# Optimization experiments

Hardware: AMD Instinct MI355X
Metric: run time of the kernel (lower is better)

## Reference

```python
import jax, jax.numpy as jnp
import numpy as np

B, C, H, W = 2, 192, 64, 64
NHEADS = 8


def setup_inputs() -> dict:
    key = jax.random.key(0)
    ks = jax.random.split(key, 6)
    L = H * W
    return {
        "x": jax.random.normal(ks[0], (B, C, H, W), dtype=jnp.float32),
        "mask": jax.random.normal(ks[1], (B, L, L), dtype=jnp.float32),
        "w_qkv": jax.random.normal(ks[2], (3 * C, C), dtype=jnp.float32) * (1.0 / np.sqrt(C)),
        "b_qkv": jax.random.normal(ks[3], (3 * C,), dtype=jnp.float32) * 0.02,
        "w_proj": jax.random.normal(ks[4], (C, C), dtype=jnp.float32) * (1.0 / np.sqrt(C)),
        "b_proj": jax.random.normal(ks[5], (C,), dtype=jnp.float32) * 0.02,
        "num_heads": NHEADS,
    }


def reference(x, mask, w_qkv, b_qkv, w_proj, b_proj, num_heads):
    b, c, h, w = x.shape
    L = h * w
    hd = c // num_heads  # head dim
    # 1x1 conv == per-pixel linear over channels
    qkv = jnp.einsum('bchw,oc->bohw', x, w_qkv) + b_qkv[None, :, None, None]
    q, k, v = jnp.split(qkv, 3, axis=1)  # each [b, c, h, w]

    def to_heads(t):
        # b (head hd) h w -> b head (h w) hd
        return t.reshape(b, num_heads, hd, L).transpose(0, 1, 3, 2)

    q, k, v = to_heads(q), to_heads(k), to_heads(v)
    scale = num_heads ** (-0.5)  # NOTE: original scales by num_heads, not head_dim
    attn = jnp.einsum('bnld,bnmd->bnlm', q, k) * scale + mask[:, None, :, :]
    attn = jax.nn.softmax(attn, axis=-1)
    out = jnp.einsum('bnlm,bnmd->bnld', attn, v)  # [b, head, L, hd]
    # b head L hd -> b (head hd) h w
    out = out.transpose(0, 1, 3, 2).reshape(b, c, h, w)
    out = jnp.einsum('bchw,oc->bohw', out, w_proj) + b_proj[None, :, None, None]
    return out
```

## Files before the change

### kernel.cpp

```cpp
#include <hip/hip_runtime.h>

#define B_  2
#define C_  192
#define L_  4096
#define NH_ 8
#define HD_ 24
#define C3_ 576
#define KV_ 64
#define NT_ (L_ / KV_)

typedef _Float16 f16;
typedef __attribute__((ext_vector_type(8))) f16 f16x8;
typedef __attribute__((ext_vector_type(16))) float f32x16;

__device__ __forceinline__ int pk2(float a, float b) {
    union { __fp16 h __attribute__((ext_vector_type(2))); int i; } u;
    u.h = __builtin_amdgcn_cvt_pkrtz(a, b);
    return u.i;
}
__device__ __forceinline__ int pk2_rte(float a, float b) {
    union { f16 h[2]; int i; } u;
    u.h[0] = (f16)a; u.h[1] = (f16)b;
    return u.i;
}

union Frag { f16x8 v; int i[4]; };

#define MFMA32(A, Bx, Cc) __builtin_amdgcn_mfma_f32_32x32x16_f16((A), (Bx), (Cc), 0, 0, 0)

__device__ __forceinline__ void gload4(const void* g, void* lds) {
    typedef const unsigned int __attribute__((address_space(1))) as1u;
    typedef unsigned int __attribute__((address_space(3))) as3u;
    __builtin_amdgcn_global_load_lds((as1u*)g,
                                     (as3u*)(unsigned int)(unsigned long long)lds,
                                     4, 0, 0);
}

__global__ __launch_bounds__(256) void lin_qkv(const float* __restrict__ a,
                                               const float* __restrict__ w,
                                               const float* __restrict__ bias,
                                               unsigned int* __restrict__ q2,
                                               unsigned int* __restrict__ k2,
                                               unsigned short* __restrict__ v16) {
    __shared__ float wl[8][C_];
    const int og  = blockIdx.x;
    const int b   = blockIdx.y >> 4;
    const int lt  = blockIdx.y & 15;
    const int tid = threadIdx.x;

    for (int e = tid; e < 8 * C_; e += 256) wl[e / C_][e % C_] = w[og * 8 * C_ + e];
    __syncthreads();

    const int l = lt * 256 + tid;
    float acc[8];
#pragma unroll
    for (int j = 0; j < 8; ++j) acc[j] = bias[og * 8 + j];

    const float* ap = a + (size_t)b * C_ * L_ + l;
#pragma unroll 2
    for (int c = 0; c < C_; ++c) {
        const float xv = ap[(size_t)c * L_];
#pragma unroll
        for (int j = 0; j < 8; ++j) acc[j] = fmaf(wl[j][c], xv, acc[j]);
    }

    const float scale = 0.35355339059327373f;
    if (og < 48) {
        unsigned int* dst = (og < 24) ? q2 : k2;
        const int og_ = (og < 24) ? og : og - 24;
        const float sc = (og < 24) ? scale : 1.f;
        const int h = og_ / 3, j0 = (og_ % 3) * 4;
        unsigned int* p = dst + ((size_t)(b * NH_ + h) * 12 + j0) * L_ + l;
#pragma unroll
        for (int j = 0; j < 4; ++j)
            p[(size_t)j * L_] = pk2_rte(acc[2 * j] * sc, acc[2 * j + 1] * sc);
    } else {
        const int og_ = og - 48;
        const int h = og_ / 3, d0 = (og_ % 3) * 8;
        unsigned short* p = v16 + ((size_t)(b * NH_ + h) * 24 + d0) * L_ + l;
#pragma unroll
        for (int j = 0; j < 8; ++j) {
            union { f16 hf; unsigned short us; } cv;
            cv.hf = (f16)acc[j];
            p[(size_t)j * L_] = cv.us;
        }
    }
}

__global__ __launch_bounds__(256) void lin_kernel(const float* __restrict__ a,
                                                  const float* __restrict__ w,
                                                  const float* __restrict__ bias,
                                                  float* __restrict__ out, int OC) {
    __shared__ float wl[8][C_];
    const int og  = blockIdx.x;
    const int b   = blockIdx.y >> 4;
    const int lt  = blockIdx.y & 15;
    const int tid = threadIdx.x;

    for (int e = tid; e < 8 * C_; e += 256) wl[e / C_][e % C_] = w[og * 8 * C_ + e];
    __syncthreads();

    const int l = lt * 256 + tid;
    float acc[8];
#pragma unroll
    for (int j = 0; j < 8; ++j) acc[j] = bias[og * 8 + j];

    const float* ap = a + (size_t)b * C_ * L_ + l;
#pragma unroll 2
    for (int c = 0; c < C_; ++c) {
        const float xv = ap[(size_t)c * L_];
#pragma unroll
        for (int j = 0; j < 8; ++j) acc[j] = fmaf(wl[j][c], xv, acc[j]);
    }

    float* op = out + ((size_t)b * OC + og * 8) * L_ + l;
#pragma unroll
    for (int j = 0; j < 8; ++j) op[(size_t)j * L_] = acc[j];
}

__global__ __launch_bounds__(256) void attn_mfma(const unsigned int* __restrict__ q2,
                                                 const unsigned int* __restrict__ k2,
                                                 const unsigned short* __restrict__ v16,
                                                 const float* __restrict__ mask,
                                                 float* __restrict__ out) {
    const int tid  = threadIdx.x;
    const int lane = tid & 63;
    const int wid  = tid >> 6;
    const int hi   = lane >> 5;
    const int lq   = lane & 31;
    const int bid  = blockIdx.x;
    const int h    = bid >> 6;
    const int b    = (bid >> 5) & 1;
    const int qt   = bid & 31;
    const int qrow = qt * 128 + wid * 32 + lq;

    __shared__ int k_lds[2][16][64];
    __shared__ int v_lds[2][32][32];

    {
        const int r = 12 + (tid >> 6), c0 = tid & 63;
        k_lds[0][r][c0] = 0;
        k_lds[1][r][c0] = 0;
    }

    const unsigned int*   qb = q2  + (size_t)(b * NH_ + h) * 12 * L_;
    const unsigned int*   kb = k2  + (size_t)(b * NH_ + h) * 12 * L_;
    const unsigned short* vb = v16 + (size_t)(b * NH_ + h) * 24 * L_;
    const float* mrow = mask + ((size_t)b * L_ + qrow) * L_;

    int bq[8];
#pragma unroll
    for (int s = 0; s < 2; ++s)
#pragma unroll
        for (int t = 0; t < 4; ++t) {
            const int dpq = 8 * s + 4 * hi + t;
            bq[s * 4 + t] = (dpq < 12) ? qb[(size_t)dpq * L_ + qrow] : 0;
        }

    const unsigned int*   kg[3];
    const unsigned short* vg[3];
    int kls[3], vls[3];
#pragma unroll
    for (int i = 0; i < 3; ++i) {
        const int e = i * 256 + tid;
        kg[i]  = kb + (size_t)(e >> 6) * L_ + (e & 63);
        kls[i] = i * 256 + 64 * wid;
        const int d = e >> 5, slot = e & 31;
        vg[i]  = vb + (size_t)d * L_ + 2 * (slot ^ d);
        vls[i] = i * 256 + 64 * wid;
    }

#define STAGE(BUF, KK) do {                                                   \
    _Pragma("unroll")                                                         \
    for (int i_ = 0; i_ < 3; ++i_) {                                          \
        gload4(kg[i_] + (KK), &k_lds[BUF][0][0] + kls[i_]);                   \
        gload4(vg[i_] + (KK), &v_lds[BUF][0][0] + vls[i_]);                   \
    } } while (0)

#define MLOAD(MD, KK) do {                                                    \
    const float4* mb_ = (const float4*)(mrow + (KK));                         \
    _Pragma("unroll")                                                         \
    for (int u_ = 0; u_ < 2; ++u_)                                            \
        _Pragma("unroll")                                                     \
        for (int q_ = 0; q_ < 4; ++q_)                                        \
            MD[u_ * 4 + q_] = mb_[8 * u_ + 2 * q_ + hi];                      \
    } while (0)

#define PVSTEP(CU, U) do {                                                    \
    int w1[4], w2[4], s1[4], s2[4];                                           \
    _Pragma("unroll")                                                         \
    for (int q_ = 0; q_ < 4; ++q_) {                                          \
        w1[q_] = pk2(CU[4 * q_], CU[4 * q_ + 1]);                             \
        w2[q_] = pk2(CU[4 * q_ + 2], CU[4 * q_ + 3]);                         \
    }                                                                         \
    _Pragma("unroll")                                                         \
    for (int q_ = 0; q_ < 4; ++q_) {                                          \
        s1[q_] = __shfl_xor(w1[q_], 32);                                      \
        s2[q_] = __shfl_xor(w2[q_], 32);                                      \
    }                                                                         \
    _Pragma("unroll")                                                         \
    for (int s_ = 0; s_ < 2; ++s_) {                                          \
        const int qq_ = 2 * s_ + hi;                                          \
        Frag pb, va;                                                          \
        pb.i[0] = hi ? s1[qq_] : w1[qq_];                                     \
        pb.i[1] = hi ? s2[qq_] : w2[qq_];                                     \
        pb.i[2] = hi ? w1[qq_] : s1[qq_];                                     \
        pb.i[3] = hi ? w2[qq_] : s2[qq_];                                     \
        _Pragma("unroll")                                                     \
        for (int t_ = 0; t_ < 4; ++t_)                                        \
            va.i[t_] = v_lds[BUF_ACTIVE][lq][(16 * U + 8 * s_ + 4 * hi + t_) ^ lq]; \
        o = MFMA32(va.v, pb.v, o);                                            \
    } } while (0)

#define COMPUTE(BUF, MC) do {                                                 \
    const int BUF_ACTIVE = (BUF);                                             \
    f32x16 c0, c1;                                                            \
    c0[0] = MC[0].x; c0[1] = MC[0].y; c0[2]  = MC[0].z; c0[3]  = MC[0].w;     \
    c0[4] = MC[1].x; c0[5] = MC[1].y; c0[6]  = MC[1].z; c0[7]  = MC[1].w;     \
    c0[8] = MC[2].x; c0[9] = MC[2].y; c0[10] = MC[2].z; c0[11] = MC[2].w;     \
    c0[12] = MC[3].x; c0[13] = MC[3].y; c0[14] = MC[3].z; c0[15] = MC[3].w;   \
    c1[0] = MC[4].x; c1[1] = MC[4].y; c1[2]  = MC[4].z; c1[3]  = MC[4].w;     \
    c1[4] = MC[5].x; c1[5] = MC[5].y; c1[6]  = MC[5].z; c1[7]  = MC[5].w;     \
    c1[8] = MC[6].x; c1[9] = MC[6].y; c1[10] = MC[6].z; c1[11] = MC[6].w;     \
    c1[12] = MC[7].x; c1[13] = MC[7].y; c1[14] = MC[7].z; c1[15] = MC[7].w;   \
    Frag qf0, qf1, ka0, ka1;                                                  \
    _Pragma("unroll")                                                         \
    for (int t_ = 0; t_ < 4; ++t_) { qf0.i[t_] = bq[t_]; qf1.i[t_] = bq[4 + t_]; } \
    _Pragma("unroll")                                                         \
    for (int t_ = 0; t_ < 4; ++t_) {                                          \
        ka0.i[t_] = k_lds[BUF_ACTIVE][4 * hi + t_][lq];                       \
        ka1.i[t_] = k_lds[BUF_ACTIVE][8 + 4 * hi + t_][lq];                   \
    }                                                                         \
    c0 = MFMA32(ka0.v, qf0.v, c0);                                            \
    c0 = MFMA32(ka1.v, qf1.v, c0);                                            \
    _Pragma("unroll")                                                         \
    for (int t_ = 0; t_ < 4; ++t_) {                                          \
        ka0.i[t_] = k_lds[BUF_ACTIVE][4 * hi + t_][32 + lq];                  \
        ka1.i[t_] = k_lds[BUF_ACTIVE][8 + 4 * hi + t_][32 + lq];              \
    }                                                                         \
    c1 = MFMA32(ka0.v, qf0.v, c1);                                            \
    c1 = MFMA32(ka1.v, qf1.v, c1);                                            \
    float pmax = c0[0];                                                       \
    _Pragma("unroll")                                                         \
    for (int i_ = 1; i_ < 16; ++i_) pmax = fmaxf(pmax, c0[i_]);               \
    _Pragma("unroll")                                                         \
    for (int i_ = 0; i_ < 16; ++i_) pmax = fmaxf(pmax, c1[i_]);               \
    pmax = fmaxf(pmax, __shfl_xor(pmax, 32));                                 \
    if (!__all(pmax <= mrun + 8.f)) {                                         \
        const float newm_ = fmaxf(mrun, pmax);                                \
        const float r_ = __expf(mrun - newm_);                                \
        srun *= r_;                                                           \
        _Pragma("unroll")                                                     \
        for (int i_ = 0; i_ < 16; ++i_) o[i_] *= r_;                          \
        mrun = newm_;                                                         \
    }                                                                         \
    float ls = 0.f;                                                           \
    _Pragma("unroll")                                                         \
    for (int i_ = 0; i_ < 16; ++i_) { c0[i_] = __expf(c0[i_] - mrun); ls += c0[i_]; } \
    _Pragma("unroll")                                                         \
    for (int i_ = 0; i_ < 16; ++i_) { c1[i_] = __expf(c1[i_] - mrun); ls += c1[i_]; } \
    ls += __shfl_xor(ls, 32);                                                 \
    srun += ls;                                                               \
    PVSTEP(c0, 0);                                                            \
    PVSTEP(c1, 1);                                                            \
    } while (0)

    f32x16 o;
#pragma unroll
    for (int i = 0; i < 16; ++i) o[i] = 0.f;
    float mrun = -1e30f, srun = 0.f;
    float4 mc[8], mn[8];

    STAGE(0, 0);
    MLOAD(mc, 0);
    __syncthreads();

    for (int t = 0; t < NT_; t += 2) {
        const int kk = t * KV_;
        STAGE(1, kk + KV_);
        MLOAD(mn, kk + KV_);
        COMPUTE(0, mc);
        __syncthreads();
        if (t + 2 < NT_) {
            STAGE(0, kk + 2 * KV_);
            MLOAD(mc, kk + 2 * KV_);
        }
        COMPUTE(1, mn);
        __syncthreads();
    }

    const float inv = 1.f / srun;
    float* op = out + ((size_t)b * C_ + h * HD_) * L_ + qrow;
#pragma unroll
    for (int i = 0; i < 16; ++i) {
        const int d = (i & 3) + 8 * (i >> 2) + 4 * hi;
        if (d < HD_) op[(size_t)d * L_] = o[i] * inv;
    }
#undef STAGE
#undef MLOAD
#undef PVSTEP
#undef COMPUTE
}

extern "C" void kernel_launch(void* const* d_in, const int* in_sizes, int n_in,
                              void* d_out, int out_size, void* d_ws, size_t ws_size,
                              hipStream_t stream) {
    const float* x      = (const float*)d_in[0];
    const float* mask   = (const float*)d_in[1];
    const float* w_qkv  = (const float*)d_in[2];
    const float* b_qkv  = (const float*)d_in[3];
    const float* w_proj = (const float*)d_in[4];
    const float* b_proj = (const float*)d_in[5];
    float* out = (float*)d_out;

    unsigned int*   q2  = (unsigned int*)d_ws;
    unsigned int*   k2  = q2 + (size_t)B_ * NH_ * 12 * L_;
    unsigned short* v16 = (unsigned short*)(k2 + (size_t)B_ * NH_ * 12 * L_);
    float* ws_att = (float*)(v16 + (size_t)B_ * NH_ * 24 * L_);

    lin_qkv<<<dim3(72, 32), 256, 0, stream>>>(x, w_qkv, b_qkv, q2, k2, v16);
    attn_mfma<<<dim3(512), 256, 0, stream>>>(q2, k2, v16, mask, ws_att);
    lin_kernel<<<dim3(24, 32), 256, 0, stream>>>(ws_att, w_proj, b_proj, out, C_);
}
```

Before: 344.7 us.

## Deepen attention K/V pipeline to four LDS buffers with exp2 softmax

Replaces the double-buffered K/V staging, which called __syncthreads each tile, with a four-deep LDS ring. Loads are issued two tiles ahead and waited on with explicit vmcnt counts plus raw barriers, so the wave does not drain all outstanding loads. Softmax moves to base 2: log2(e) is folded into the q scale and the mask, and the exponentials use v_exp_f32 directly. The MFMAs are wrapped with s_setprio. The hand-counted vmcnt waits and the LDS buffer reuse are fragile and could race if the count of in-flight loads differs from what was assumed.

After: 371.6 us. 1.08x slower.

```diff
diff --git a/kernel.cpp b/kernel.cpp
--- a/kernel.cpp
+++ b/kernel.cpp
@@ -13,6 +13,8 @@
 typedef __attribute__((ext_vector_type(8))) f16 f16x8;
 typedef __attribute__((ext_vector_type(16))) float f32x16;
 
+#define L2E_ 1.4426950408889634f
+
 __device__ __forceinline__ int pk2(float a, float b) {
     union { __fp16 h __attribute__((ext_vector_type(2))); int i; } u;
     u.h = __builtin_amdgcn_cvt_pkrtz(a, b);
@@ -22,6 +24,11 @@
     union { f16 h[2]; int i; } u;
     u.h[0] = (f16)a; u.h[1] = (f16)b;
     return u.i;
+}
+__device__ __forceinline__ float ex2(float x) {
+    float r;
+    asm("v_exp_f32 %0, %1" : "=v"(r) : "v"(x));
+    return r;
 }
 
 union Frag { f16x8 v; int i[4]; };
@@ -35,6 +42,9 @@
                                      (as3u*)(unsigned int)(unsigned long long)lds,
                                      4, 0, 0);
 }
+
+#define WAITV(N) asm volatile("s_waitcnt vmcnt(" #N ")" ::: "memory")
+#define BAR()    __builtin_amdgcn_s_barrier()
 
 __global__ __launch_bounds__(256) void lin_qkv(const float* __restrict__ a,
                                                const float* __restrict__ w,
@@ -64,11 +74,11 @@
         for (int j = 0; j < 8; ++j) acc[j] = fmaf(wl[j][c], xv, acc[j]);
     }
 
-    const float scale = 0.35355339059327373f;
+    const float qscale = 0.35355339059327373f * L2E_;
     if (og < 48) {
         unsigned int* dst = (og < 24) ? q2 : k2;
         const int og_ = (og < 24) ? og : og - 24;
-        const float sc = (og < 24) ? scale : 1.f;
+        const float sc = (og < 24) ? qscale : 1.f;
         const int h = og_ / 3, j0 = (og_ % 3) * 4;
         unsigned int* p = dst + ((size_t)(b * NH_ + h) * 12 + j0) * L_ + l;
 #pragma unroll
@@ -134,14 +144,13 @@
     const int qt   = bid & 31;
     const int qrow = qt * 128 + wid * 32 + lq;
 
-    __shared__ int k_lds[2][16][64];
-    __shared__ int v_lds[2][32][32];
-
-    {
-        const int r = 12 + (tid >> 6), c0 = tid & 63;
-        k_lds[0][r][c0] = 0;
-        k_lds[1][r][c0] = 0;
-    }
+    __shared__ int k_lds[4][16][64];
+    __shared__ int v_lds[4][32][32];
+
+#pragma unroll
+    for (int bf = 0; bf < 4; ++bf)
+#pragma unroll
+        for (int i = 0; i < 4; ++i) k_lds[bf][12 + i][lane] = 0;
 
     const unsigned int*   qb = q2  + (size_t)(b * NH_ + h) * 12 * L_;
     const unsigned int*   kb = k2  + (size_t)(b * NH_ + h) * 12 * L_;
@@ -159,22 +168,21 @@
 
     const unsigned int*   kg[3];
     const unsigned short* vg[3];
-    int kls[3], vls[3];
+    int ls_off[3];
 #pragma unroll
     for (int i = 0; i < 3; ++i) {
         const int e = i * 256 + tid;
-        kg[i]  = kb + (size_t)(e >> 6) * L_ + (e & 63);
-        kls[i] = i * 256 + 64 * wid;
+        kg[i]     = kb + (size_t)(e >> 6) * L_ + (e & 63);
         const int d = e >> 5, slot = e & 31;
-        vg[i]  = vb + (size_t)d * L_ + 2 * (slot ^ d);
-        vls[i] = i * 256 + 64 * wid;
-    }
-
-#define STAGE(BUF, KK) do {                                                   \
+        vg[i]     = vb + (size_t)d * L_ + 2 * (slot ^ d);
+        ls_off[i] = i * 256 + 64 * wid;
+    }
+
+#define STAGE(BF, KK) do {                                                    \
     _Pragma("unroll")                                                         \
     for (int i_ = 0; i_ < 3; ++i_) {                                          \
-        gload4(kg[i_] + (KK), &k_lds[BUF][0][0] + kls[i_]);                   \
-        gload4(vg[i_] + (KK), &v_lds[BUF][0][0] + vls[i_]);                   \
+        gload4(kg[i_] + (KK), &k_lds[BF][0][0] + ls_off[i_]);                 \
+        gload4(vg[i_] + (KK), &v_lds[BF][0][0] + ls_off[i_]);                 \
     } } while (0)
 
 #define MLOAD(MD, KK) do {                                                    \
@@ -186,7 +194,7 @@
             MD[u_ * 4 + q_] = mb_[8 * u_ + 2 * q_ + hi];                      \
     } while (0)
 
-#define PVSTEP(CU, U) do {                                                    \
+#define PVSTEP(BF, CU, U) do {                                                \
     int w1[4], w2[4], s1[4], s2[4];                                           \
     _Pragma("unroll")                                                         \
     for (int q_ = 0; q_ < 4; ++q_) {                                          \
@@ -208,47 +216,60 @@
         pb.i[3] = hi ? w2[qq_] : s2[qq_];                                     \
         _Pragma("unroll")                                                     \
         for (int t_ = 0; t_ < 4; ++t_)                                        \
-            va.i[t_] = v_lds[BUF_ACTIVE][lq][(16 * U + 8 * s_ + 4 * hi + t_) ^ lq]; \
+            va.i[t_] = v_lds[BF][lq][(16 * U + 8 * s_ + 4 * hi + t_) ^ lq];   \
+        __builtin_amdgcn_s_setprio(1);                                        \
         o = MFMA32(va.v, pb.v, o);                                            \
+        __builtin_amdgcn_s_setprio(0);                                        \
     } } while (0)
 
-#define COMPUTE(BUF, MC) do {                                                 \
-    const int BUF_ACTIVE = (BUF);                                             \
+#define COMPUTE(BF, MC) do {                                                  \
     f32x16 c0, c1;                                                            \
-    c0[0] = MC[0].x; c0[1] = MC[0].y; c0[2]  = MC[0].z; c0[3]  = MC[0].w;     \
-    c0[4] = MC[1].x; c0[5] = MC[1].y; c0[6]  = MC[1].z; c0[7]  = MC[1].w;     \
-    c0[8] = MC[2].x; c0[9] = MC[2].y; c0[10] = MC[2].z; c0[11] = MC[2].w;     \
-    c0[12] = MC[3].x; c0[13] = MC[3].y; c0[14] = MC[3].z; c0[15] = MC[3].w;   \
-    c1[0] = MC[4].x; c1[1] = MC[4].y; c1[2]  = MC[4].z; c1[3]  = MC[4].w;     \
-    c1[4] = MC[5].x; c1[5] = MC[5].y; c1[6]  = MC[5].z; c1[7]  = MC[5].w;     \
-    c1[8] = MC[6].x; c1[9] = MC[6].y; c1[10] = MC[6].z; c1[11] = MC[6].w;     \
-    c1[12] = MC[7].x; c1[13] = MC[7].y; c1[14] = MC[7].z; c1[15] = MC[7].w;   \
+    c0[0]  = MC[0].x * L2E_; c0[1]  = MC[0].y * L2E_;                         \
+    c0[2]  = MC[0].z * L2E_; c0[3]  = MC[0].w * L2E_;                         \
+    c0[4]  = MC[1].x * L2E_; c0[5]  = MC[1].y * L2E_;                         \
+    c0[6]  = MC[1].z * L2E_; c0[7]  = MC[1].w * L2E_;                         \
+    c0[8]  = MC[2].x * L2E_; c0[9]  = MC[2].y * L2E_;                         \
+    c0[10] = MC[2].z * L2E_; c0[11] = MC[2].w * L2E_;                         \
+    c0[12] = MC[3].x * L2E_; c0[13] = MC[3].y * L2E_;                         \
+    c0[14] = MC[3].z * L2E_; c0[15] = MC[3].w * L2E_;                         \
+    c1[0]  = MC[4].x * L2E_; c1[1]  = MC[4].y * L2E_;                         \
+    c1[2]  = MC[4].z * L2E_; c1[3]  = MC[4].w * L2E_;                         \
+    c1[4]  = MC[5].x * L2E_; c1[5]  = MC[5].y * L2E_;                         \
+    c1[6]  = MC[5].z * L2E_; c1[7]  = MC[5].w * L2E_;                         \
+    c1[8]  = MC[6].x * L2E_; c1[9]  = MC[6].y * L2E_;                         \
+    c1[10] = MC[6].z * L2E_; c1[11] = MC[6].w * L2E_;                         \
+    c1[12] = MC[7].x * L2E_; c1[13] = MC[7].y * L2E_;                         \
+    c1[14] = MC[7].z * L2E_; c1[15] = MC[7].w * L2E_;                         \
     Frag qf0, qf1, ka0, ka1;                                                  \
     _Pragma("unroll")                                                         \
     for (int t_ = 0; t_ < 4; ++t_) { qf0.i[t_] = bq[t_]; qf1.i[t_] = bq[4 + t_]; } \
     _Pragma("unroll")                                                         \
     for (int t_ = 0; t_ < 4; ++t_) {                                          \
-        ka0.i[t_] = k_lds[BUF_ACTIVE][4 * hi + t_][lq];                       \
-        ka1.i[t_] = k_lds[BUF_ACTIVE][8 + 4 * hi + t_][lq];                   \
-    }                                                                         \
+        ka0.i[t_] = k_lds[BF][4 * hi + t_][lq];                               \
+        ka1.i[t_] = k_lds[BF][8 + 4 * hi + t_][lq];                           \
+    }                                                                         \
+    __builtin_amdgcn_s_setprio(1);                                            \
     c0 = MFMA32(ka0.v, qf0.v, c0);                                            \
     c0 = MFMA32(ka1.v, qf1.v, c0);                                            \
+    __builtin_amdgcn_s_setprio(0);                                            \
     _Pragma("unroll")                                                         \
     for (int t_ = 0; t_ < 4; ++t_) {                                          \
-        ka0.i[t_] = k_lds[BUF_ACTIVE][4 * hi + t_][32 + lq];                  \
-        ka1.i[t_] = k_lds[BUF_ACTIVE][8 + 4 * hi + t_][32 + lq];              \
-    }                                                                         \
+        ka0.i[t_] = k_lds[BF][4 * hi + t_][32 + lq];                          \
+        ka1.i[t_] = k_lds[BF][8 + 4 * hi + t_][32 + lq];                      \
+    }                                                                         \
+    __builtin_amdgcn_s_setprio(1);                                            \
     c1 = MFMA32(ka0.v, qf0.v, c1);                                            \
     c1 = MFMA32(ka1.v, qf1.v, c1);                                            \
+    __builtin_amdgcn_s_setprio(0);                                            \
     float pmax = c0[0];                                                       \
     _Pragma("unroll")                                                         \
     for (int i_ = 1; i_ < 16; ++i_) pmax = fmaxf(pmax, c0[i_]);               \
     _Pragma("unroll")                                                         \
     for (int i_ = 0; i_ < 16; ++i_) pmax = fmaxf(pmax, c1[i_]);               \
     pmax = fmaxf(pmax, __shfl_xor(pmax, 32));                                 \
-    if (!__all(pmax <= mrun + 8.f)) {                                         \
+    if (!__all((int)(pmax <= mrun + 11.5415603f))) {                          \
         const float newm_ = fmaxf(mrun, pmax);                                \
-        const float r_ = __expf(mrun - newm_);                                \
+        const float r_ = ex2(mrun - newm_);                                   \
         srun *= r_;                                                           \
         _Pragma("unroll")                                                     \
         for (int i_ = 0; i_ < 16; ++i_) o[i_] *= r_;                          \
@@ -256,37 +277,39 @@
     }                                                                         \
     float ls = 0.f;                                                           \
     _Pragma("unroll")                                                         \
-    for (int i_ = 0; i_ < 16; ++i_) { c0[i_] = __expf(c0[i_] - mrun); ls += c0[i_]; } \
-    _Pragma("unroll")                                                         \
-    for (int i_ = 0; i_ < 16; ++i_) { c1[i_] = __expf(c1[i_] - mrun); ls += c1[i_]; } \
+    for (int i_ = 0; i_ < 16; ++i_) { c0[i_] = ex2(c0[i_] - mrun); ls += c0[i_]; } \
+    _Pragma("unroll")                                                         \
+    for (int i_ = 0; i_ < 16; ++i_) { c1[i_] = ex2(c1[i_] - mrun); ls += c1[i_]; } \
     ls += __shfl_xor(ls, 32);                                                 \
     srun += ls;                                                               \
-    PVSTEP(c0, 0);                                                            \
-    PVSTEP(c1, 1);                                                            \
+    PVSTEP(BF, c0, 0);                                                        \
+    PVSTEP(BF, c1, 1);                                                        \
     } while (0)
 
     f32x16 o;
 #pragma unroll
     for (int i = 0; i < 16; ++i) o[i] = 0.f;
     float mrun = -1e30f, srun = 0.f;
-    float4 mc[8], mn[8];
+    float4 ma[8], mb[8];
 
     STAGE(0, 0);
-    MLOAD(mc, 0);
-    __syncthreads();
-
-    for (int t = 0; t < NT_; t += 2) {
+    MLOAD(ma, 0);
+    STAGE(1, KV_);
+
+#pragma clang loop unroll(disable)
+    for (int t = 0; t < NT_ - 4; t += 4) {
         const int kk = t * KV_;
-        STAGE(1, kk + KV_);
-        MLOAD(mn, kk + KV_);
-        COMPUTE(0, mc);
-        __syncthreads();
-        if (t + 2 < NT_) {
-            STAGE(0, kk + 2 * KV_);
-            MLOAD(mc, kk + 2 * KV_);
-        }
-        COMPUTE(1, mn);
-        __syncthreads();
+        MLOAD(mb, kk + 1 * KV_); STAGE(2, kk + 2 * KV_); WAITV(20); BAR(); COMPUTE(0, ma);
+        MLOAD(ma, kk + 2 * KV_); STAGE(3, kk + 3 * KV_); WAITV(20); BAR(); COMPUTE(1, mb);
+        MLOAD(mb, kk + 3 * KV_); STAGE(0, kk + 4 * KV_); WAITV(20); BAR(); COMPUTE(2, ma);
+        MLOAD(ma, kk + 4 * KV_); STAGE(1, kk + 5 * KV_); WAITV(20); BAR(); COMPUTE(3, mb);
+    }
+    {
+        const int kk = (NT_ - 4) * KV_;
+        MLOAD(mb, kk + 1 * KV_); STAGE(2, kk + 2 * KV_); WAITV(20); BAR(); COMPUTE(0, ma);
+        MLOAD(ma, kk + 2 * KV_); STAGE(3, kk + 3 * KV_); WAITV(20); BAR(); COMPUTE(1, mb);
+        MLOAD(mb, kk + 3 * KV_);                         WAITV(14); BAR(); COMPUTE(2, ma);
+                                                         WAITV(0);  BAR(); COMPUTE(3, mb);
     }
 
     const float inv = 1.f / srun;
```
